# Kernel tuning notes

Measured on AMD Instinct MI355X. Metric: run time of the kernel, lower is better.

## Reference

```python
import jax, jax.numpy as jnp
import numpy as np

SPIKING_T = 8        # args['spiking_t']
V_TH = 1.0           # spikingjelly IFNode default v_threshold
TAU = 2.0            # NonSpikingLIFNode tau
ALPHA = 4.0          # spikingjelly default Sigmoid surrogate alpha
MIN_LOG_STD, MAX_LOG_STD = -20.0, 2.0
LOG_2PI = float(np.log(2.0 * np.pi))

@jax.custom_vjp
def spike(x):
    # Heaviside forward (spikingjelly surrogate.Sigmoid behavior)
    return (x >= 0.0).astype(x.dtype)

def _spike_fwd(x):
    return spike(x), x

def _spike_bwd(x, g):
    s = jax.nn.sigmoid(ALPHA * x)
    return (g * ALPHA * s * (1.0 - s),)

spike.defvjp(_spike_fwd, _spike_bwd)


def setup_inputs() -> dict:
    key = jax.random.key(0)
    ks = jax.random.split(key, 8)
    B, N, H, A = 8192, 128, 1024, 32
    def lin_w(k, fan_in, fan_out):
        return jax.random.normal(k, (fan_in, fan_out), dtype=jnp.float32) / jnp.sqrt(float(fan_in))
    return {
        "state": jax.random.normal(ks[0], (B, N), dtype=jnp.float32),
        "w1": lin_w(ks[1], N, H),
        "b1": jnp.full((H,), 1e-6, dtype=jnp.float32),
        "w2": lin_w(ks[2], H, H),
        "b2": jnp.full((H,), 1e-6, dtype=jnp.float32),
        "w3": lin_w(ks[3], H, 2 * A),
        "b3": jnp.full((2 * A,), 1e-6, dtype=jnp.float32),
        "eps": jax.random.normal(ks[4], (B, A), dtype=jnp.float32),
    }


def reference(state, w1, b1, w2, b2, w3, b3, eps):
    B = state.shape[0]
    H = w1.shape[1]
    O = w3.shape[1]
    v1 = jnp.zeros((B, H), state.dtype)
    v2 = jnp.zeros((B, H), state.dtype)
    v3 = jnp.zeros((B, O), state.dtype)

    def step(carry, _):
        v1, v2, v3 = carry
        # IF node 1: charge, fire, hard reset to 0
        h1 = v1 + state @ w1 + b1
        s1 = spike(h1 - V_TH)
        v1 = h1 * (1.0 - s1)
        # IF node 2
        h2 = v2 + s1 @ w2 + b2
        s2 = spike(h2 - V_TH)
        v2 = h2 * (1.0 - s2)
        # NonSpiking LIF (decay_input=True, v_reset=0): v += (x - v)/tau
        x3 = s2 @ w3 + b3
        v3 = v3 + (x3 - v3) / TAU
        return (v1, v2, v3), None

    (v1, v2, v3), _ = jax.lax.scan(step, (v1, v2, v3), None, length=SPIKING_T)

    mu, log_std = jnp.split(v3, 2, axis=-1)
    log_std = jnp.clip(log_std, MIN_LOG_STD, MAX_LOG_STD)
    std = jnp.exp(log_std)
    z = mu + std * eps            # Normal rsample
    action = jnp.tanh(z)
    # Normal(mu, std).log_prob(z) = -eps^2/2 - log_std - 0.5*log(2*pi)
    log_prob = (-0.5 * eps * eps - log_std - 0.5 * LOG_2PI) \
               - jnp.log(1.0 - action * action + 1e-7)
    log_prob = jnp.sum(log_prob, axis=-1, keepdims=True)
    return action, log_prob
```

## Files before the change

### kernel.cpp

```cpp
#include <hip/hip_runtime.h>

typedef float    f32x4 __attribute__((ext_vector_type(4)));
typedef int      i32x4 __attribute__((ext_vector_type(4)));
typedef unsigned u32x4 __attribute__((ext_vector_type(4)));

typedef const __attribute__((address_space(1))) void* gptr_t;
typedef __attribute__((address_space(3))) void* lptr_t;

__device__ __forceinline__ void gload_lds16(const void* g, void* l) {
  __builtin_amdgcn_global_load_lds((gptr_t)g, (lptr_t)l, 16, 0, 0);
}

constexpr int Bsz  = 8192;
constexpr int Nin  = 128;
constexpr int Hd   = 1024;
constexpr int Aact = 32;
constexpr int Od   = 64;
constexpr int KC = 384;
constexpr float DELTA = 1.5e-4f;
constexpr unsigned WCAP = 262144;

__global__ void wsplit_all_kernel(const float* __restrict__ w2, const float* __restrict__ w3,
                                  char* __restrict__ p1, char* __restrict__ p2,
                                  char* __restrict__ p3,
                                  char* __restrict__ r1, char* __restrict__ r2,
                                  char* __restrict__ r3,
                                  float* __restrict__ w2tf) {
  const int lane = threadIdx.x;
  const int l15 = lane & 15, quad = lane >> 4;
  const int pn = blockIdx.x;
  const int kb = blockIdx.y;
  const bool isw3 = (pn >= Hd / 16);
  const int pnl = isw3 ? pn - Hd / 16 : pn;
  const float* src = isw3 ? w3 : w2;
  const int N = isw3 ? Od : Hd;
  const int n = pnl * 16 + l15;
  const int k0 = kb * 64 + quad * 16;
  char* d1 = isw3 ? r1 : p1;
  char* d2 = isw3 ? r2 : p2;
  char* d3 = isw3 ? r3 : p3;
  float wv[16];
  char o1[16], o2[16], o3[16];
#pragma unroll
  for (int e = 0; e < 16; ++e) {
    float w = src[(size_t)(k0 + e) * N + n];
    wv[e] = w;
    float m1 = rintf(w * 512.0f);
    float q1 = w - m1 * (1.0f / 512.0f);
    float m2 = rintf(q1 * 65536.0f);
    float q2 = q1 - m2 * (1.0f / 65536.0f);
    float m3 = rintf(q2 * 8388608.0f);
    o1[e] = (char)(int)m1; o2[e] = (char)(int)m2; o3[e] = (char)(int)m3;
  }
  size_t off = ((size_t)pnl * 16 + kb) * 1024 + (size_t)lane * 16;
#pragma unroll
  for (int e = 0; e < 16; ++e) {
    d1[off + e] = o1[e]; d2[off + e] = o2[e]; d3[off + e] = o3[e];
  }
  if (!isw3) {
#pragma unroll
    for (int e = 0; e < 16; ++e)
      w2tf[(size_t)n * Hd + k0 + e] = wv[e];
  }
}

__global__ __launch_bounds__(256)
void x1_kernel(const float* __restrict__ state, const float* __restrict__ w1,
               const float* __restrict__ b1, unsigned char* __restrict__ s1pack) {
  __shared__ float sA[64][129];
  __shared__ float sB[128][68];
  const int m0 = blockIdx.x * 64, n0 = blockIdx.y * 64;
  const int tid = threadIdx.x;
  for (int idx = tid; idx < 64 * 32; idx += 256) {
    int r = idx >> 5, c4 = (idx & 31) << 2;
    float4 v = *(const float4*)(state + (size_t)(m0 + r) * Nin + c4);
    sA[r][c4] = v.x; sA[r][c4 + 1] = v.y; sA[r][c4 + 2] = v.z; sA[r][c4 + 3] = v.w;
  }
  for (int idx = tid; idx < 128 * 16; idx += 256) {
    int r = idx >> 4, c4 = (idx & 15) << 2;
    *(float4*)&sB[r][c4] = *(const float4*)(w1 + (size_t)r * Hd + n0 + c4);
  }
  __syncthreads();
  const int tx = tid & 15, ty = tid >> 4;
  float acc[4][4] = {};
  for (int k = 0; k < 128; ++k) {
    float a[4];
#pragma unroll
    for (int i = 0; i < 4; ++i) a[i] = sA[ty * 4 + i][k];
    float4 b = *(const float4*)&sB[k][tx * 4];
#pragma unroll
    for (int i = 0; i < 4; ++i) {
      acc[i][0] = __fmaf_rn(a[i], b.x, acc[i][0]);
      acc[i][1] = __fmaf_rn(a[i], b.y, acc[i][1]);
      acc[i][2] = __fmaf_rn(a[i], b.z, acc[i][2]);
      acc[i][3] = __fmaf_rn(a[i], b.w, acc[i][3]);
    }
  }
#pragma unroll
  for (int i = 0; i < 4; ++i) {
    int m = m0 + ty * 4 + i;
    unsigned pack = 0;
#pragma unroll
    for (int j = 0; j < 4; ++j) {
      int n = n0 + tx * 4 + j;
      float x = acc[i][j];
      float bb = b1[n];
      float v = 0.0f;
      unsigned bits = 0;
#pragma unroll
      for (int t = 0; t < 8; ++t) {
        float h = __fadd_rn(__fadd_rn(v, x), bb);
        if (h >= 1.0f) { bits |= (1u << t); v = 0.0f; } else { v = h; }
      }
      pack |= bits << (8 * j);
    }
    *(unsigned*)(s1pack + (size_t)m * Hd + n0 + tx * 4) = pack;
  }
}

__global__ __launch_bounds__(256, 3)
void gemm2i8_kernel(const unsigned char* __restrict__ s1pack,
                    const char* __restrict__ q1, const char* __restrict__ q2,
                    const char* __restrict__ q3,
                    const float* __restrict__ b2,
                    unsigned char* __restrict__ s2p,
                    unsigned* __restrict__ wcnt, unsigned* __restrict__ wlist) {
  constexpr int NKB = Hd / 64;
  constexpr int NPH = NKB / 2;
  __shared__ __align__(16) unsigned char lA[6][64 * 64];
  __shared__ __align__(16) char lB[6][3072];
  const int tid = threadIdx.x;
  const int m0 = blockIdx.x * 64;
  const int n0 = blockIdx.y * 16;
  const int wave = tid >> 6, lane = tid & 63, l15 = lane & 15, quad = lane >> 4;
  const char* bplane = (wave == 0) ? q1 : (wave == 1) ? q2 : q3;
  const unsigned char* asrc = s1pack
      + (size_t)(m0 + ((tid >> 6) << 4) + (tid & 15)) * Hd + ((tid >> 4) & 3) * 16;
  const char* bsrc2 = bplane + (size_t)blockIdx.y * NKB * 1024 + (size_t)lane * 16;
  i32x4 acc[3][8] = {};

  auto stage2 = [&](int ph) {
    int t0 = 2 * ph, t1 = t0 + 1;
    gload_lds16(asrc + t0 * 64, &lA[t0 % 6][tid * 16]);
    if (wave < 3)
      gload_lds16(bsrc2 + (size_t)t0 * 1024, &lB[t0 % 6][wave * 1024 + lane * 16]);
    gload_lds16(asrc + t1 * 64, &lA[t1 % 6][tid * 16]);
    if (wave < 3)
      gload_lds16(bsrc2 + (size_t)t1 * 1024, &lB[t1 % 6][wave * 1024 + lane * 16]);
  };
  stage2(0); stage2(1);

#pragma unroll
  for (int ph = 0; ph < NPH; ++ph) {
    if (ph < NPH - 1) {
      if (wave < 3) asm volatile("s_waitcnt vmcnt(4)" ::: "memory");
      else          asm volatile("s_waitcnt vmcnt(2)" ::: "memory");
    } else {
      asm volatile("s_waitcnt vmcnt(0)" ::: "memory");
    }
    __builtin_amdgcn_s_barrier();
    asm volatile("" ::: "memory");
    const int t0 = 2 * ph, t1 = t0 + 1;
    {
      u32x4 ad = *(const u32x4*)&lA[t0 % 6][wave * 1024 + lane * 16];
      i32x4 fb0 = *(const i32x4*)&lB[t0 % 6][lane * 16];
      i32x4 fb1 = *(const i32x4*)&lB[t0 % 6][1024 + lane * 16];
      i32x4 fb2 = *(const i32x4*)&lB[t0 % 6][2048 + lane * 16];
      if (ph + 2 < NPH) stage2(ph + 2);
#pragma unroll
      for (int t = 0; t < 8; ++t) {
        i32x4 af;
        af[0] = (int)((ad[0] >> t) & 0x01010101u);
        af[1] = (int)((ad[1] >> t) & 0x01010101u);
        af[2] = (int)((ad[2] >> t) & 0x01010101u);
        af[3] = (int)((ad[3] >> t) & 0x01010101u);
        acc[0][t] = __builtin_amdgcn_mfma_i32_16x16x64_i8(af, fb0, acc[0][t], 0, 0, 0);
        acc[1][t] = __builtin_amdgcn_mfma_i32_16x16x64_i8(af, fb1, acc[1][t], 0, 0, 0);
        acc[2][t] = __builtin_amdgcn_mfma_i32_16x16x64_i8(af, fb2, acc[2][t], 0, 0, 0);
      }
    }
    {
      u32x4 ad = *(const u32x4*)&lA[t1 % 6][wave * 1024 + lane * 16];
      i32x4 fb0 = *(const i32x4*)&lB[t1 % 6][lane * 16];
      i32x4 fb1 = *(const i32x4*)&lB[t1 % 6][1024 + lane * 16];
      i32x4 fb2 = *(const i32x4*)&lB[t1 % 6][2048 + lane * 16];
#pragma unroll
      for (int t = 0; t < 8; ++t) {
        i32x4 af;
        af[0] = (int)((ad[0] >> t) & 0x01010101u);
        af[1] = (int)((ad[1] >> t) & 0x01010101u);
        af[2] = (int)((ad[2] >> t) & 0x01010101u);
        af[3] = (int)((ad[3] >> t) & 0x01010101u);
        acc[0][t] = __builtin_amdgcn_mfma_i32_16x16x64_i8(af, fb0, acc[0][t], 0, 0, 0);
        acc[1][t] = __builtin_amdgcn_mfma_i32_16x16x64_i8(af, fb1, acc[1][t], 0, 0, 0);
        acc[2][t] = __builtin_amdgcn_mfma_i32_16x16x64_i8(af, fb2, acc[2][t], 0, 0, 0);
      }
    }
  }
  const int n = n0 + l15;
  const float bb = b2[n];
#pragma unroll
  for (int r = 0; r < 4; ++r) {
    int m = m0 + wave * 16 + quad * 4 + r;
    size_t idx = (size_t)m * Hd + n;
    float v = 0.0f;
    unsigned bits = 0;
#pragma unroll
    for (int t = 0; t < 8; ++t) {
      double ge = (double)acc[0][t][r] * 1.953125e-3
                + (double)acc[1][t][r] * 1.52587890625e-5
                + (double)acc[2][t][r] * 1.1920928955078125e-7;
      float G = (float)ge;
      float h = __fadd_rn(__fadd_rn(v, G), bb);
      if (__builtin_expect(__builtin_fabsf(h - 1.0f) < DELTA, 0)) {
        unsigned pos = atomicAdd(wcnt, 1u);
        if (pos < WCAP) wlist[pos] = (unsigned)idx;
      }
      bool sp = (h >= 1.0f);
      if (sp) bits |= (1u << t);
      v = sp ? 0.0f : h;
    }
    s2p[idx] = (unsigned char)bits;
  }
}

__global__ __launch_bounds__(256)
void fixup_kernel(const unsigned* __restrict__ wcnt, const unsigned* __restrict__ wlist,
                  const unsigned char* __restrict__ s1pack, const float* __restrict__ w2tf,
                  const float* __restrict__ b2, unsigned char* __restrict__ s2p) {
  unsigned cnt = *wcnt;
  if (cnt > WCAP) cnt = WCAP;
  const int tid = threadIdx.x;
  const int lane = tid & 63;
  const int sl = lane / 3, blk3 = lane - sl * 3;
  const int wid = blockIdx.x * (blockDim.x >> 6) + (tid >> 6);
  const int nwaves = gridDim.x * (blockDim.x >> 6);
  for (unsigned base = (unsigned)wid * 21u; base < cnt; base += (unsigned)nwaves * 21u) {
    unsigned site = base + (unsigned)sl;
    bool act = (sl < 21) && (site < cnt);
    unsigned idx = act ? wlist[site] : 0u;
    int m = (int)(idx >> 10), n = (int)(idx & 1023u);
    const unsigned char* prow = s1pack + ((size_t)m << 10);
    const float* col = w2tf + ((size_t)n << 10);
    int kb = blk3 * KC;
    int kend = (blk3 == 2) ? Hd : kb + KC;
    float S[8] = {};
    if (act) {
      for (int k = kb; k < kend; k += 8) {
        float4 wa = *(const float4*)(col + k);
        float4 wb = *(const float4*)(col + k + 4);
        unsigned b0 = *(const unsigned*)(prow + k);
        unsigned b1 = *(const unsigned*)(prow + k + 4);
#pragma unroll
        for (int tau = 0; tau < 8; ++tau) {
          S[tau] = __fadd_rn(S[tau], ((b0 >> tau) & 1)        ? wa.x : 0.0f);
          S[tau] = __fadd_rn(S[tau], ((b0 >> (8 + tau)) & 1)  ? wa.y : 0.0f);
          S[tau] = __fadd_rn(S[tau], ((b0 >> (16 + tau)) & 1) ? wa.z : 0.0f);
          S[tau] = __fadd_rn(S[tau], ((b0 >> (24 + tau)) & 1) ? wa.w : 0.0f);
          S[tau] = __fadd_rn(S[tau], ((b1 >> tau) & 1)        ? wb.x : 0.0f);
          S[tau] = __fadd_rn(S[tau], ((b1 >> (8 + tau)) & 1)  ? wb.y : 0.0f);
          S[tau] = __fadd_rn(S[tau], ((b1 >> (16 + tau)) & 1) ? wb.z : 0.0f);
          S[tau] = __fadd_rn(S[tau], ((b1 >> (24 + tau)) & 1) ? wb.w : 0.0f);
        }
      }
    }
    float G[8];
#pragma unroll
    for (int tau = 0; tau < 8; ++tau) {
      float sB = __shfl(S[tau], lane + 1);
      float sC = __shfl(S[tau], lane + 2);
      G[tau] = __fadd_rn(__fadd_rn(S[tau], sB), sC);
    }
    if (act && blk3 == 0) {
      float bb = b2[n];
      float v = 0.0f;
      unsigned bits = 0;
      for (int tau = 0; tau < 8; ++tau) {
        float h = __fadd_rn(__fadd_rn(v, G[tau]), bb);
        bool sp = (h >= 1.0f);
        if (sp) bits |= (1u << tau);
        v = sp ? 0.0f : h;
      }
      s2p[idx] = (unsigned char)bits;
    }
  }
}

__global__ __launch_bounds__(256, 3)
void gemm3i8_kernel(const unsigned char* __restrict__ s2p,
                    const char* __restrict__ q1, const char* __restrict__ q2,
                    const char* __restrict__ q3,
                    const float* __restrict__ b3, float* __restrict__ v3) {
  constexpr int NKB = Hd / 64;
  constexpr int NPH = NKB / 2;
  __shared__ __align__(16) unsigned char lA[6][64 * 64];
  __shared__ __align__(16) char lB[6][3072];
  const int tid = threadIdx.x;
  const int m0 = blockIdx.x * 64;
  const int n0 = blockIdx.y * 16;
  const int wave = tid >> 6, lane = tid & 63, l15 = lane & 15, quad = lane >> 4;
  const char* bplane = (wave == 0) ? q1 : (wave == 1) ? q2 : q3;
  const unsigned char* asrc = s2p
      + (size_t)(m0 + ((tid >> 6) << 4) + (tid & 15)) * Hd + ((tid >> 4) & 3) * 16;
  const char* bsrc2 = bplane + (size_t)blockIdx.y * NKB * 1024 + (size_t)lane * 16;
  i32x4 acc[3][8] = {};

  auto stage2 = [&](int ph) {
    int t0 = 2 * ph, t1 = t0 + 1;
    gload_lds16(asrc + t0 * 64, &lA[t0 % 6][tid * 16]);
    if (wave < 3)
      gload_lds16(bsrc2 + (size_t)t0 * 1024, &lB[t0 % 6][wave * 1024 + lane * 16]);
    gload_lds16(asrc + t1 * 64, &lA[t1 % 6][tid * 16]);
    if (wave < 3)
      gload_lds16(bsrc2 + (size_t)t1 * 1024, &lB[t1 % 6][wave * 1024 + lane * 16]);
  };
  stage2(0); stage2(1);

#pragma unroll
  for (int ph = 0; ph < NPH; ++ph) {
    if (ph < NPH - 1) {
      if (wave < 3) asm volatile("s_waitcnt vmcnt(4)" ::: "memory");
      else          asm volatile("s_waitcnt vmcnt(2)" ::: "memory");
    } else {
      asm volatile("s_waitcnt vmcnt(0)" ::: "memory");
    }
    __builtin_amdgcn_s_barrier();
    asm volatile("" ::: "memory");
    const int t0 = 2 * ph, t1 = t0 + 1;
    {
      u32x4 ad = *(const u32x4*)&lA[t0 % 6][wave * 1024 + lane * 16];
      i32x4 fb0 = *(const i32x4*)&lB[t0 % 6][lane * 16];
      i32x4 fb1 = *(const i32x4*)&lB[t0 % 6][1024 + lane * 16];
      i32x4 fb2 = *(const i32x4*)&lB[t0 % 6][2048 + lane * 16];
      if (ph + 2 < NPH) stage2(ph + 2);
#pragma unroll
      for (int t = 0; t < 8; ++t) {
        i32x4 af;
        af[0] = (int)((ad[0] >> t) & 0x01010101u);
        af[1] = (int)((ad[1] >> t) & 0x01010101u);
        af[2] = (int)((ad[2] >> t) & 0x01010101u);
        af[3] = (int)((ad[3] >> t) & 0x01010101u);
        acc[0][t] = __builtin_amdgcn_mfma_i32_16x16x64_i8(af, fb0, acc[0][t], 0, 0, 0);
        acc[1][t] = __builtin_amdgcn_mfma_i32_16x16x64_i8(af, fb1, acc[1][t], 0, 0, 0);
        acc[2][t] = __builtin_amdgcn_mfma_i32_16x16x64_i8(af, fb2, acc[2][t], 0, 0, 0);
      }
    }
    {
      u32x4 ad = *(const u32x4*)&lA[t1 % 6][wave * 1024 + lane * 16];
      i32x4 fb0 = *(const i32x4*)&lB[t1 % 6][lane * 16];
      i32x4 fb1 = *(const i32x4*)&lB[t1 % 6][1024 + lane * 16];
      i32x4 fb2 = *(const i32x4*)&lB[t1 % 6][2048 + lane * 16];
#pragma unroll
      for (int t = 0; t < 8; ++t) {
        i32x4 af;
        af[0] = (int)((ad[0] >> t) & 0x01010101u);
        af[1] = (int)((ad[1] >> t) & 0x01010101u);
        af[2] = (int)((ad[2] >> t) & 0x01010101u);
        af[3] = (int)((ad[3] >> t) & 0x01010101u);
        acc[0][t] = __builtin_amdgcn_mfma_i32_16x16x64_i8(af, fb0, acc[0][t], 0, 0, 0);
        acc[1][t] = __builtin_amdgcn_mfma_i32_16x16x64_i8(af, fb1, acc[1][t], 0, 0, 0);
        acc[2][t] = __builtin_amdgcn_mfma_i32_16x16x64_i8(af, fb2, acc[2][t], 0, 0, 0);
      }
    }
  }
  const int n = n0 + l15;
  const float bb = b3[n];
#pragma unroll
  for (int r = 0; r < 4; ++r) {
    int m = m0 + wave * 16 + quad * 4 + r;
    float v = 0.0f;
#pragma unroll
    for (int t = 0; t < 8; ++t) {
      double ge = (double)acc[0][t][r] * 1.953125e-3
                + (double)acc[1][t][r] * 1.52587890625e-5
                + (double)acc[2][t][r] * 1.1920928955078125e-7;
      float x3 = __fadd_rn((float)ge, bb);
      float dd = __fsub_rn(x3, v);
      v = __fadd_rn(v, __fmul_rn(dd, 0.5f));
    }
    v3[(size_t)m * Od + n] = v;
  }
}

__global__ void final_kernel(const float* __restrict__ v3, const float* __restrict__ eps,
                             float* __restrict__ action, float* __restrict__ logp) {
  int tid = threadIdx.x;
  int row = blockIdx.x * 8 + (tid >> 5);
  int j = tid & 31;
  float mu = v3[(size_t)row * Od + j];
  float ls = v3[(size_t)row * Od + 32 + j];
  ls = fminf(fmaxf(ls, -20.0f), 2.0f);
  float sd = (float)exp((double)ls);
  float e  = eps[(size_t)row * Aact + j];
  float z  = __fadd_rn(mu, __fmul_rn(sd, e));
  float a;
  if (__builtin_fabsf(z) >= 7.90531111f) a = __builtin_copysignf(1.0f, z);
  else                                   a = (float)tanh((double)z);
  float aa = __fmul_rn(a, a);
  float u  = __fadd_rn(__fsub_rn(1.0f, aa), 1e-7f);
  float lg = (float)log((double)u);
  float l  = __fmul_rn(__fmul_rn(-0.5f, e), e);
  l = __fsub_rn(l, ls);
  l = __fsub_rn(l, 0.9189385332046727f);
  float term = __fsub_rn(l, lg);
  action[(size_t)row * Aact + j] = a;
  double lp = (double)term;
#pragma unroll
  for (int w = 16; w >= 1; w >>= 1) lp += __shfl_xor(lp, w);
  if (j == 0) logp[row] = (float)lp;
}

extern "C" void kernel_launch(void* const* d_in, const int* in_sizes, int n_in,
                              void* d_out, int out_size, void* d_ws, size_t ws_size,
                              hipStream_t stream) {
  const float* state = (const float*)d_in[0];
  const float* w1 = (const float*)d_in[1];
  const float* b1 = (const float*)d_in[2];
  const float* w2 = (const float*)d_in[3];
  const float* b2 = (const float*)d_in[4];
  const float* w3 = (const float*)d_in[5];
  const float* b3 = (const float*)d_in[6];
  const float* eps = (const float*)d_in[7];
  float* out_action = (float*)d_out;
  float* out_logp = out_action + (size_t)Bsz * Aact;

  char* p = (char*)d_ws;
  auto take = [&](size_t bytes) {
    char* r = p;
    p += (bytes + 255) & ~(size_t)255;
    return r;
  };
  float* v3f = (float*)take((size_t)Bsz * Od * 4);
  unsigned char* s1pack = (unsigned char*)take((size_t)Bsz * Hd);
  unsigned char* s2p = (unsigned char*)take((size_t)Bsz * Hd);
  char* w2q1 = (char*)take((size_t)Hd * Hd);
  char* w2q2 = (char*)take((size_t)Hd * Hd);
  char* w2q3 = (char*)take((size_t)Hd * Hd);
  char* w3q1 = (char*)take((size_t)Hd * Od);
  char* w3q2 = (char*)take((size_t)Hd * Od);
  char* w3q3 = (char*)take((size_t)Hd * Od);
  float* w2tf = (float*)take((size_t)Hd * Hd * 4);
  unsigned* wcnt = (unsigned*)take(8 * 4);
  unsigned* wlist = (unsigned*)take((size_t)WCAP * 4);

  wsplit_all_kernel<<<dim3(Hd / 16 + Od / 16, Hd / 64), 64, 0, stream>>>(
      w2, w3, w2q1, w2q2, w2q3, w3q1, w3q2, w3q3, w2tf);
  x1_kernel<<<dim3(Bsz / 64, Hd / 64), 256, 0, stream>>>(state, w1, b1, s1pack);
  hipMemsetAsync(wcnt, 0, 8 * 4, stream);

  gemm2i8_kernel<<<dim3(Bsz / 64, Hd / 16), 256, 0, stream>>>(s1pack, w2q1, w2q2, w2q3,
                                                              b2, s2p, wcnt, wlist);
  fixup_kernel<<<128, 256, 0, stream>>>(wcnt, wlist, s1pack, w2tf, b2, s2p);

  gemm3i8_kernel<<<dim3(Bsz / 64, Od / 16), 256, 0, stream>>>(s2p, w3q1, w3q2, w3q3,
                                                              b3, v3f);
  final_kernel<<<Bsz / 8, 256, 0, stream>>>(v3f, eps, out_action, out_logp);
}
```

Before: 320.2 us.

## Replace LDS-staged pipeline with direct register prefetch in int8 GEMM kernels

Both the layer-2 and layer-3 int8 MFMA GEMM kernels drop the six-slot LDS ring buffer fed by global_load_lds, along with its waitcnt and barrier sync. Each wave now loads its A spike-bit tile and all three B weight planes straight from global memory into registers, prefetching one k-block ahead. This removes LDS traffic, barriers and LDS occupancy limits. In exchange each wave reloads the shared B planes itself, where before they were loaded once and shared through LDS, and the prefetch is shallower.

```diff
diff --git a/kernel.cpp b/kernel.cpp
--- a/kernel.cpp
+++ b/kernel.cpp
@@ -3,13 +3,6 @@
 typedef float    f32x4 __attribute__((ext_vector_type(4)));
 typedef int      i32x4 __attribute__((ext_vector_type(4)));
 typedef unsigned u32x4 __attribute__((ext_vector_type(4)));
-
-typedef const __attribute__((address_space(1))) void* gptr_t;
-typedef __attribute__((address_space(3))) void* lptr_t;
-
-__device__ __forceinline__ void gload_lds16(const void* g, void* l) {
-  __builtin_amdgcn_global_load_lds((gptr_t)g, (lptr_t)l, 16, 0, 0);
-}
 
 constexpr int Bsz  = 8192;
 constexpr int Nin  = 128;
@@ -126,76 +119,43 @@
                     unsigned char* __restrict__ s2p,
                     unsigned* __restrict__ wcnt, unsigned* __restrict__ wlist) {
   constexpr int NKB = Hd / 64;
-  constexpr int NPH = NKB / 2;
-  __shared__ __align__(16) unsigned char lA[6][64 * 64];
-  __shared__ __align__(16) char lB[6][3072];
   const int tid = threadIdx.x;
   const int m0 = blockIdx.x * 64;
   const int n0 = blockIdx.y * 16;
   const int wave = tid >> 6, lane = tid & 63, l15 = lane & 15, quad = lane >> 4;
-  const char* bplane = (wave == 0) ? q1 : (wave == 1) ? q2 : q3;
   const unsigned char* asrc = s1pack
-      + (size_t)(m0 + ((tid >> 6) << 4) + (tid & 15)) * Hd + ((tid >> 4) & 3) * 16;
-  const char* bsrc2 = bplane + (size_t)blockIdx.y * NKB * 1024 + (size_t)lane * 16;
+      + (size_t)(m0 + wave * 16 + l15) * Hd + (lane >> 4) * 16;
+  const size_t boff = (size_t)blockIdx.y * NKB * 1024 + (size_t)lane * 16;
+  const char* bp0 = q1 + boff;
+  const char* bp1 = q2 + boff;
+  const char* bp2 = q3 + boff;
   i32x4 acc[3][8] = {};
 
-  auto stage2 = [&](int ph) {
-    int t0 = 2 * ph, t1 = t0 + 1;
-    gload_lds16(asrc + t0 * 64, &lA[t0 % 6][tid * 16]);
-    if (wave < 3)
-      gload_lds16(bsrc2 + (size_t)t0 * 1024, &lB[t0 % 6][wave * 1024 + lane * 16]);
-    gload_lds16(asrc + t1 * 64, &lA[t1 % 6][tid * 16]);
-    if (wave < 3)
-      gload_lds16(bsrc2 + (size_t)t1 * 1024, &lB[t1 % 6][wave * 1024 + lane * 16]);
-  };
-  stage2(0); stage2(1);
-
-#pragma unroll
-  for (int ph = 0; ph < NPH; ++ph) {
-    if (ph < NPH - 1) {
-      if (wave < 3) asm volatile("s_waitcnt vmcnt(4)" ::: "memory");
-      else          asm volatile("s_waitcnt vmcnt(2)" ::: "memory");
-    } else {
-      asm volatile("s_waitcnt vmcnt(0)" ::: "memory");
-    }
-    __builtin_amdgcn_s_barrier();
-    asm volatile("" ::: "memory");
-    const int t0 = 2 * ph, t1 = t0 + 1;
-    {
-      u32x4 ad = *(const u32x4*)&lA[t0 % 6][wave * 1024 + lane * 16];
-      i32x4 fb0 = *(const i32x4*)&lB[t0 % 6][lane * 16];
-      i32x4 fb1 = *(const i32x4*)&lB[t0 % 6][1024 + lane * 16];
-      i32x4 fb2 = *(const i32x4*)&lB[t0 % 6][2048 + lane * 16];
-      if (ph + 2 < NPH) stage2(ph + 2);
-#pragma unroll
-      for (int t = 0; t < 8; ++t) {
-        i32x4 af;
-        af[0] = (int)((ad[0] >> t) & 0x01010101u);
-        af[1] = (int)((ad[1] >> t) & 0x01010101u);
-        af[2] = (int)((ad[2] >> t) & 0x01010101u);
-        af[3] = (int)((ad[3] >> t) & 0x01010101u);
-        acc[0][t] = __builtin_amdgcn_mfma_i32_16x16x64_i8(af, fb0, acc[0][t], 0, 0, 0);
-        acc[1][t] = __builtin_amdgcn_mfma_i32_16x16x64_i8(af, fb1, acc[1][t], 0, 0, 0);
-        acc[2][t] = __builtin_amdgcn_mfma_i32_16x16x64_i8(af, fb2, acc[2][t], 0, 0, 0);
-      }
-    }
-    {
-      u32x4 ad = *(const u32x4*)&lA[t1 % 6][wave * 1024 + lane * 16];
-      i32x4 fb0 = *(const i32x4*)&lB[t1 % 6][lane * 16];
-      i32x4 fb1 = *(const i32x4*)&lB[t1 % 6][1024 + lane * 16];
-      i32x4 fb2 = *(const i32x4*)&lB[t1 % 6][2048 + lane * 16];
-#pragma unroll
-      for (int t = 0; t < 8; ++t) {
-        i32x4 af;
-        af[0] = (int)((ad[0] >> t) & 0x01010101u);
-        af[1] = (int)((ad[1] >> t) & 0x01010101u);
-        af[2] = (int)((ad[2] >> t) & 0x01010101u);
-        af[3] = (int)((ad[3] >> t) & 0x01010101u);
-        acc[0][t] = __builtin_amdgcn_mfma_i32_16x16x64_i8(af, fb0, acc[0][t], 0, 0, 0);
-        acc[1][t] = __builtin_amdgcn_mfma_i32_16x16x64_i8(af, fb1, acc[1][t], 0, 0, 0);
-        acc[2][t] = __builtin_amdgcn_mfma_i32_16x16x64_i8(af, fb2, acc[2][t], 0, 0, 0);
-      }
-    }
+  u32x4 a_cur = *(const u32x4*)asrc;
+  i32x4 f0c = *(const i32x4*)bp0;
+  i32x4 f1c = *(const i32x4*)bp1;
+  i32x4 f2c = *(const i32x4*)bp2;
+#pragma unroll
+  for (int kb = 0; kb < NKB; ++kb) {
+    u32x4 a_nxt = a_cur; i32x4 f0n = f0c, f1n = f1c, f2n = f2c;
+    if (kb + 1 < NKB) {
+      a_nxt = *(const u32x4*)(asrc + (kb + 1) * 64);
+      f0n = *(const i32x4*)(bp0 + (size_t)(kb + 1) * 1024);
+      f1n = *(const i32x4*)(bp1 + (size_t)(kb + 1) * 1024);
+      f2n = *(const i32x4*)(bp2 + (size_t)(kb + 1) * 1024);
+    }
+#pragma unroll
+    for (int t = 0; t < 8; ++t) {
+      i32x4 af;
+      af[0] = (int)((a_cur[0] >> t) & 0x01010101u);
+      af[1] = (int)((a_cur[1] >> t) & 0x01010101u);
+      af[2] = (int)((a_cur[2] >> t) & 0x01010101u);
+      af[3] = (int)((a_cur[3] >> t) & 0x01010101u);
+      acc[0][t] = __builtin_amdgcn_mfma_i32_16x16x64_i8(af, f0c, acc[0][t], 0, 0, 0);
+      acc[1][t] = __builtin_amdgcn_mfma_i32_16x16x64_i8(af, f1c, acc[1][t], 0, 0, 0);
+      acc[2][t] = __builtin_amdgcn_mfma_i32_16x16x64_i8(af, f2c, acc[2][t], 0, 0, 0);
+    }
+    a_cur = a_nxt; f0c = f0n; f1c = f1n; f2c = f2n;
   }
   const int n = n0 + l15;
   const float bb = b2[n];
@@ -292,76 +252,43 @@
                     const char* __restrict__ q3,
                     const float* __restrict__ b3, float* __restrict__ v3) {
   constexpr int NKB = Hd / 64;
-  constexpr int NPH = NKB / 2;
-  __shared__ __align__(16) unsigned char lA[6][64 * 64];
-  __shared__ __align__(16) char lB[6][3072];
   const int tid = threadIdx.x;
   const int m0 = blockIdx.x * 64;
   const int n0 = blockIdx.y * 16;
   const int wave = tid >> 6, lane = tid & 63, l15 = lane & 15, quad = lane >> 4;
-  const char* bplane = (wave == 0) ? q1 : (wave == 1) ? q2 : q3;
   const unsigned char* asrc = s2p
-      + (size_t)(m0 + ((tid >> 6) << 4) + (tid & 15)) * Hd + ((tid >> 4) & 3) * 16;
-  const char* bsrc2 = bplane + (size_t)blockIdx.y * NKB * 1024 + (size_t)lane * 16;
+      + (size_t)(m0 + wave * 16 + l15) * Hd + (lane >> 4) * 16;
+  const size_t boff = (size_t)blockIdx.y * NKB * 1024 + (size_t)lane * 16;
+  const char* bp0 = q1 + boff;
+  const char* bp1 = q2 + boff;
+  const char* bp2 = q3 + boff;
   i32x4 acc[3][8] = {};
 
-  auto stage2 = [&](int ph) {
-    int t0 = 2 * ph, t1 = t0 + 1;
-    gload_lds16(asrc + t0 * 64, &lA[t0 % 6][tid * 16]);
-    if (wave < 3)
-      gload_lds16(bsrc2 + (size_t)t0 * 1024, &lB[t0 % 6][wave * 1024 + lane * 16]);
-    gload_lds16(asrc + t1 * 64, &lA[t1 % 6][tid * 16]);
-    if (wave < 3)
-      gload_lds16(bsrc2 + (size_t)t1 * 1024, &lB[t1 % 6][wave * 1024 + lane * 16]);
-  };
-  stage2(0); stage2(1);
-
-#pragma unroll
-  for (int ph = 0; ph < NPH; ++ph) {
-    if (ph < NPH - 1) {
-      if (wave < 3) asm volatile("s_waitcnt vmcnt(4)" ::: "memory");
-      else          asm volatile("s_waitcnt vmcnt(2)" ::: "memory");
-    } else {
-      asm volatile("s_waitcnt vmcnt(0)" ::: "memory");
-    }
-    __builtin_amdgcn_s_barrier();
-    asm volatile("" ::: "memory");
-    const int t0 = 2 * ph, t1 = t0 + 1;
-    {
-      u32x4 ad = *(const u32x4*)&lA[t0 % 6][wave * 1024 + lane * 16];
-      i32x4 fb0 = *(const i32x4*)&lB[t0 % 6][lane * 16];
-      i32x4 fb1 = *(const i32x4*)&lB[t0 % 6][1024 + lane * 16];
-      i32x4 fb2 = *(const i32x4*)&lB[t0 % 6][2048 + lane * 16];
-      if (ph + 2 < NPH) stage2(ph + 2);
-#pragma unroll
-      for (int t = 0; t < 8; ++t) {
-        i32x4 af;
-        af[0] = (int)((ad[0] >> t) & 0x01010101u);
-        af[1] = (int)((ad[1] >> t) & 0x01010101u);
-        af[2] = (int)((ad[2] >> t) & 0x01010101u);
-        af[3] = (int)((ad[3] >> t) & 0x01010101u);
-        acc[0][t] = __builtin_amdgcn_mfma_i32_16x16x64_i8(af, fb0, acc[0][t], 0, 0, 0);
-        acc[1][t] = __builtin_amdgcn_mfma_i32_16x16x64_i8(af, fb1, acc[1][t], 0, 0, 0);
-        acc[2][t] = __builtin_amdgcn_mfma_i32_16x16x64_i8(af, fb2, acc[2][t], 0, 0, 0);
-      }
-    }
-    {
-      u32x4 ad = *(const u32x4*)&lA[t1 % 6][wave * 1024 + lane * 16];
-      i32x4 fb0 = *(const i32x4*)&lB[t1 % 6][lane * 16];
-      i32x4 fb1 = *(const i32x4*)&lB[t1 % 6][1024 + lane * 16];
-      i32x4 fb2 = *(const i32x4*)&lB[t1 % 6][2048 + lane * 16];
-#pragma unroll
-      for (int t = 0; t < 8; ++t) {
-        i32x4 af;
-        af[0] = (int)((ad[0] >> t) & 0x01010101u);
-        af[1] = (int)((ad[1] >> t) & 0x01010101u);
-        af[2] = (int)((ad[2] >> t) & 0x01010101u);
-        af[3] = (int)((ad[3] >> t) & 0x01010101u);
-        acc[0][t] = __builtin_amdgcn_mfma_i32_16x16x64_i8(af, fb0, acc[0][t], 0, 0, 0);
-        acc[1][t] = __builtin_amdgcn_mfma_i32_16x16x64_i8(af, fb1, acc[1][t], 0, 0, 0);
-        acc[2][t] = __builtin_amdgcn_mfma_i32_16x16x64_i8(af, fb2, acc[2][t], 0, 0, 0);
-      }
-    }
+  u32x4 a_cur = *(const u32x4*)asrc;
+  i32x4 f0c = *(const i32x4*)bp0;
+  i32x4 f1c = *(const i32x4*)bp1;
+  i32x4 f2c = *(const i32x4*)bp2;
+#pragma unroll
+  for (int kb = 0; kb < NKB; ++kb) {
+    u32x4 a_nxt = a_cur; i32x4 f0n = f0c, f1n = f1c, f2n = f2c;
+    if (kb + 1 < NKB) {
+      a_nxt = *(const u32x4*)(asrc + (kb + 1) * 64);
+      f0n = *(const i32x4*)(bp0 + (size_t)(kb + 1) * 1024);
+      f1n = *(const i32x4*)(bp1 + (size_t)(kb + 1) * 1024);
+      f2n = *(const i32x4*)(bp2 + (size_t)(kb + 1) * 1024);
+    }
+#pragma unroll
+    for (int t = 0; t < 8; ++t) {
+      i32x4 af;
+      af[0] = (int)((a_cur[0] >> t) & 0x01010101u);
+      af[1] = (int)((a_cur[1] >> t) & 0x01010101u);
+      af[2] = (int)((a_cur[2] >> t) & 0x01010101u);
+      af[3] = (int)((a_cur[3] >> t) & 0x01010101u);
+      acc[0][t] = __builtin_amdgcn_mfma_i32_16x16x64_i8(af, f0c, acc[0][t], 0, 0, 0);
+      acc[1][t] = __builtin_amdgcn_mfma_i32_16x16x64_i8(af, f1c, acc[1][t], 0, 0, 0);
+      acc[2][t] = __builtin_amdgcn_mfma_i32_16x16x64_i8(af, f2c, acc[2][t], 0, 0, 0);
+    }
+    a_cur = a_nxt; f0c = f0n; f1c = f1n; f2c = f2n;
   }
   const int n = n0 + l15;
   const float bb = b3[n];
```

Result: no change. 325.9 us (+1.8%).
